# Performance work log

Measured on AMD Instinct MI355X. Metric: run time of the kernel, lower is better.

## Reference

```python
import jax, jax.numpy as jnp
import numpy as np

N = 1024
T = 8
HID = 256
FD = 64
SB = 8  # agents per sub-batch
EPS = 1e-6


def setup_inputs() -> dict:
    key = jax.random.key(0)
    ks = jax.random.split(key, 12)
    s = 0.05
    starts = jnp.arange(0, N, SB)
    sub_batches = jnp.stack([starts, starts + SB], axis=1).astype(jnp.int64)  # [128,2]
    return {
        'in_xy': jax.random.normal(ks[0], (T, N, 2), jnp.float32),
        'in_dxdy': jax.random.normal(ks[1], (T, N, 2), jnp.float32),
        'enc_h': jax.random.normal(ks[2], (N, HID), jnp.float32),
        'sub_batches': sub_batches,
        'W1': jax.random.normal(ks[3], (3, 32), jnp.float32) * s,
        'b1': jnp.zeros((32,), jnp.float32),
        'W2': jax.random.normal(ks[4], (32, 64), jnp.float32) * s,
        'b2': jnp.zeros((64,), jnp.float32),
        'W3': jax.random.normal(ks[5], (64, FD), jnp.float32) * s,
        'b3': jnp.zeros((FD,), jnp.float32),
        'Wa': jax.random.normal(ks[6], (HID, FD), jnp.float32) * s,
        'ba': jnp.zeros((FD,), jnp.float32),
    }


def _social_attention(in_xy, in_dxdy, enc_h, sub_batches, W1, b1, W2, b2, W3, b3, Wa, ba):
    x4 = jnp.concatenate([in_xy[-1], in_dxdy[-1]], axis=-1)  # [N,4] pos+vel
    # pairwise differences Dx[i,j] = x[i] - x[j]
    D = x4[:, None, :] - x4[None, :, :]                      # [N,N,4]
    Dp, Dv = D[..., :2], D[..., 2:]
    l2 = jnp.linalg.norm(Dp, axis=2)                         # [N,N]
    v = x4[:, 2:]                                            # [N,2] velocity of i
    dot_dp_v = Dp[..., 0] * v[:, None, 0] + Dp[..., 1] * v[:, None, 1]
    cos_theta = dot_dp_v / (l2 * jnp.linalg.norm(v, axis=1)[:, None] + EPS)
    dot_pv = jnp.sum(Dp * Dv, axis=-1)
    dv_sq = jnp.sum(Dv * Dv, axis=-1) + EPS
    ttca = -dot_pv / dv_sq
    dca = jnp.linalg.norm(Dp + ttca[..., None] * Dv, axis=2)
    feats = jnp.stack([l2, cos_theta, dca], axis=-1)         # [N,N,3]
    # social feature embedding MLP 3->32->64->FD
    h1 = jax.nn.relu(feats @ W1 + b1)
    h2 = jax.nn.relu(h1 @ W2 + b2)
    f = h2 @ W3 + b3                                         # [N,N,FD]
    # attention pooling, segmented by sub-batches with masked diagonal
    Wh = enc_h @ Wa + ba                                     # [N,FD]
    sigma = jnp.einsum('ijf,jf->ij', f, Wh)                  # [N,N]
    n = enc_h.shape[0]
    idx = jnp.arange(n)
    seg_id = jnp.searchsorted(sub_batches[:, 0], idx, side='right') - 1  # [N]
    same_seg = seg_id[:, None] == seg_id[None, :]
    diag = idx[:, None] == idx[None, :]
    score = jnp.where(diag, jnp.float32(-1000.0), sigma)
    score = jnp.where(same_seg, score, -jnp.inf)
    att = jax.nn.softmax(score, axis=1)                      # [N,N]
    S = att @ enc_h                                          # [N,HID]
    sizes = sub_batches[:, 1] - sub_batches[:, 0]
    keep = (sizes[seg_id] > 1)[:, None]
    return jnp.where(keep, S, jnp.float32(0.0))


def reference(in_xy, in_dxdy, enc_h, sub_batches, W1, b1, W2, b2, W3, b3, Wa, ba):
    return _social_attention(in_xy, in_dxdy, enc_h, sub_batches,
                             W1, b1, W2, b2, W3, b3, Wa, ba)
```

## Files before the change

### kernel.cpp

```cpp
#include <hip/hip_runtime.h>
#include <math.h>

#define NN    1024
#define TT    8
#define HIDD  256
#define FDD   64
#define SBB   8
#define EPSF  1e-6f
#define W3PAD 68
#define GPAD  68

__global__ __launch_bounds__(512) void social_attn_kernel(
    const float* __restrict__ in_xy,
    const float* __restrict__ in_dxdy,
    const float* __restrict__ enc_h,
    const float* __restrict__ W1, const float* __restrict__ b1,
    const float* __restrict__ W2, const float* __restrict__ b2,
    const float* __restrict__ W3, const float* __restrict__ b3,
    const float* __restrict__ Wa, const float* __restrict__ ba,
    float* __restrict__ out)
{
    __shared__ float sW1[96];
    __shared__ float sb1[32];
    __shared__ float sW2[32 * 64];
    __shared__ float sb2[64];
    __shared__ float sb3[64];
    __shared__ float sW3P[64 * W3PAD];
    __shared__ float sEnc[SBB * HIDD];
    __shared__ float sWh[SBB * FDD];
    __shared__ float sG[SBB * GPAD];
    __shared__ float sG0[SBB];
    __shared__ float sPsig[SBB * 64];
    __shared__ float sAtt[64];
    __shared__ float sX4[SBB][4];

    const int t    = threadIdx.x;
    const int wv   = t >> 6;
    const int lane = t & 63;
    const int seg  = blockIdx.x;
    const int base = seg * SBB;

    if (t < 96)        sW1[t]        = W1[t];
    else if (t < 128)  sb1[t - 96]   = b1[t - 96];
    else if (t < 192)  sb2[t - 128]  = b2[t - 128];
    else if (t < 256)  sb3[t - 192]  = b3[t - 192];
    ((float4*)sW2)[t] = ((const float4*)W2)[t];
    #pragma unroll
    for (int k = 0; k < 8; ++k) {
        const int idx = t + k * 512;
        sW3P[(idx >> 6) * W3PAD + (idx & 63)] = W3[idx];
    }
    ((float4*)sEnc)[t] = ((const float4*)(enc_h + (size_t)base * HIDD))[t];
    if (t < SBB) {
        const int g = base + t;
        const float* xy   = in_xy   + (TT - 1) * NN * 2;
        const float* dxdy = in_dxdy + (TT - 1) * NN * 2;
        sX4[t][0] = xy[2 * g];
        sX4[t][1] = xy[2 * g + 1];
        sX4[t][2] = dxdy[2 * g];
        sX4[t][3] = dxdy[2 * g + 1];
    }
    __syncthreads();

    const int cs = lane >> 4, k4 = lane & 15;
    float4 wacc = make_float4(0.f, 0.f, 0.f, 0.f);
    #pragma unroll 8
    for (int c2 = 0; c2 < 64; ++c2) {
        const int c = cs * 64 + ((c2 + 8 * cs) & 63);
        const float  e  = sEnc[wv * HIDD + c];
        const float4 wa = *(const float4*)&Wa[c * FDD + k4 * 4];
        wacc.x = fmaf(e, wa.x, wacc.x);
        wacc.y = fmaf(e, wa.y, wacc.y);
        wacc.z = fmaf(e, wa.z, wacc.z);
        wacc.w = fmaf(e, wa.w, wacc.w);
    }
    wacc.x += __shfl_xor(wacc.x, 16, 64);
    wacc.y += __shfl_xor(wacc.y, 16, 64);
    wacc.z += __shfl_xor(wacc.z, 16, 64);
    wacc.w += __shfl_xor(wacc.w, 16, 64);
    wacc.x += __shfl_xor(wacc.x, 32, 64);
    wacc.y += __shfl_xor(wacc.y, 32, 64);
    wacc.z += __shfl_xor(wacc.z, 32, 64);
    wacc.w += __shfl_xor(wacc.w, 32, 64);
    if (lane < 16) {
        const float4 bav = *(const float4*)&ba[k4 * 4];
        wacc.x += bav.x; wacc.y += bav.y; wacc.z += bav.z; wacc.w += bav.w;
        *(float4*)&sWh[wv * FDD + k4 * 4] = wacc;
    }

    float gacc = 0.f;
    #pragma unroll
    for (int c4 = 0; c4 < 16; ++c4) {
        const float4 w3 = *(const float4*)&sW3P[lane * W3PAD + c4 * 4];
        const float4 wh = *(const float4*)&sWh[wv * FDD + c4 * 4];
        gacc = fmaf(w3.x, wh.x, gacc);
        gacc = fmaf(w3.y, wh.y, gacc);
        gacc = fmaf(w3.z, wh.z, gacc);
        gacc = fmaf(w3.w, wh.w, gacc);
    }
    sG[wv * GPAD + lane] = gacc;
    float g0p = sb3[lane] * sWh[wv * FDD + lane];
    #pragma unroll
    for (int d = 1; d < 64; d <<= 1) g0p += __shfl_xor(g0p, d, 64);
    if (lane == 0) sG0[wv] = g0p;

    const int p = lane, i = p >> 3, j = p & 7, u = wv;
    const float dpx = sX4[i][0] - sX4[j][0];
    const float dpy = sX4[i][1] - sX4[j][1];
    const float dvx = sX4[i][2] - sX4[j][2];
    const float dvy = sX4[i][3] - sX4[j][3];
    const float l2  = sqrtf(dpx * dpx + dpy * dpy);
    const float vx  = sX4[i][2], vy = sX4[i][3];
    const float vnorm = sqrtf(vx * vx + vy * vy);
    const float cos_theta = (dpx * vx + dpy * vy) / (l2 * vnorm + EPSF);
    const float dot_pv = dpx * dvx + dpy * dvy;
    const float dv_sq  = dvx * dvx + dvy * dvy + EPSF;
    const float ttca   = -dot_pv / dv_sq;
    const float ex = dpx + ttca * dvx;
    const float ey = dpy + ttca * dvy;
    const float dca = sqrtf(ex * ex + ey * ey);

    float h1[32];
    #pragma unroll
    for (int c = 0; c < 32; ++c) {
        float a = sb1[c];
        a = fmaf(l2,        sW1[c],      a);
        a = fmaf(cos_theta, sW1[32 + c], a);
        a = fmaf(dca,       sW1[64 + c], a);
        h1[c] = a > 0.f ? a : 0.f;
    }

    float f2[8];
    #pragma unroll
    for (int cc = 0; cc < 8; ++cc) f2[cc] = sb2[u * 8 + cc];
    #pragma unroll
    for (int r = 0; r < 32; ++r) {
        const float hr = h1[r];
        const float4 wa = *(const float4*)&sW2[r * 64 + u * 8];
        const float4 wb = *(const float4*)&sW2[r * 64 + u * 8 + 4];
        f2[0] = fmaf(hr, wa.x, f2[0]);
        f2[1] = fmaf(hr, wa.y, f2[1]);
        f2[2] = fmaf(hr, wa.z, f2[2]);
        f2[3] = fmaf(hr, wa.w, f2[3]);
        f2[4] = fmaf(hr, wb.x, f2[4]);
        f2[5] = fmaf(hr, wb.y, f2[5]);
        f2[6] = fmaf(hr, wb.z, f2[6]);
        f2[7] = fmaf(hr, wb.w, f2[7]);
    }
    #pragma unroll
    for (int cc = 0; cc < 8; ++cc) f2[cc] = fmaxf(f2[cc], 0.f);
    __syncthreads();

    const float4 ga = *(const float4*)&sG[j * GPAD + u * 8];
    const float4 gb = *(const float4*)&sG[j * GPAD + u * 8 + 4];
    float psig;
    psig = f2[0] * ga.x;
    psig = fmaf(f2[1], ga.y, psig);
    psig = fmaf(f2[2], ga.z, psig);
    psig = fmaf(f2[3], ga.w, psig);
    psig = fmaf(f2[4], gb.x, psig);
    psig = fmaf(f2[5], gb.y, psig);
    psig = fmaf(f2[6], gb.z, psig);
    psig = fmaf(f2[7], gb.w, psig);
    sPsig[u * 64 + p] = psig;
    __syncthreads();

    float tot = sG0[j];
    #pragma unroll
    for (int uu = 0; uu < 8; ++uu) tot += sPsig[uu * 64 + lane];
    const float score = (i == j) ? -1000.f : tot;
    float m = score;
    m = fmaxf(m, __shfl_xor(m, 1, 64));
    m = fmaxf(m, __shfl_xor(m, 2, 64));
    m = fmaxf(m, __shfl_xor(m, 4, 64));
    const float e = expf(score - m);
    float ssum = e;
    ssum += __shfl_xor(ssum, 1, 64);
    ssum += __shfl_xor(ssum, 2, 64);
    ssum += __shfl_xor(ssum, 4, 64);
    if (t < 64) sAtt[lane] = e / ssum;
    __syncthreads();

    float4 acc4 = make_float4(0.f, 0.f, 0.f, 0.f);
    #pragma unroll
    for (int j2 = 0; j2 < 8; ++j2) {
        const float  a  = sAtt[wv * 8 + j2];
        const float4 ev = *(const float4*)&sEnc[j2 * HIDD + lane * 4];
        acc4.x = fmaf(a, ev.x, acc4.x);
        acc4.y = fmaf(a, ev.y, acc4.y);
        acc4.z = fmaf(a, ev.z, acc4.z);
        acc4.w = fmaf(a, ev.w, acc4.w);
    }
    *(float4*)&out[(size_t)(base + wv) * HIDD + lane * 4] = acc4;
}

extern "C" void kernel_launch(void* const* d_in, const int* in_sizes, int n_in,
                              void* d_out, int out_size, void* d_ws, size_t ws_size,
                              hipStream_t stream) {
    const float* in_xy   = (const float*)d_in[0];
    const float* in_dxdy = (const float*)d_in[1];
    const float* enc_h   = (const float*)d_in[2];
    const float* W1 = (const float*)d_in[4];
    const float* b1 = (const float*)d_in[5];
    const float* W2 = (const float*)d_in[6];
    const float* b2 = (const float*)d_in[7];
    const float* W3 = (const float*)d_in[8];
    const float* b3 = (const float*)d_in[9];
    const float* Wa = (const float*)d_in[10];
    const float* ba = (const float*)d_in[11];

    social_attn_kernel<<<NN / SBB, 512, 0, stream>>>(
        in_xy, in_dxdy, enc_h, W1, b1, W2, b2, W3, b3, Wa, ba, (float*)d_out);
}
```

Before: 13.97 us.

## Give each wave one query agent so scoring and softmax stay in registers

Work is remapped so each wave owns one query agent i. Lanes hold the neighbour j and a chunk of eight output channels, and the sigma reduction uses intra-wave shuffles instead of a shared-memory partial-sum array. This removes two __syncthreads barriers and the sPsig/sAtt shared buffers, and attention weights are broadcast with __shfl. Wh is also computed by reading enc_h directly from global memory before the first barrier, so it can overlap the shared-memory staging. In exchange, every wave now recomputes the pairwise features and the 3->32 MLP layer, and the Wh loop makes uncoalesced global reads.

After: 15.12 us. +8.2%, slower.

```diff
diff --git a/kernel.cpp b/kernel.cpp
--- a/kernel.cpp
+++ b/kernel.cpp
@@ -30,8 +30,6 @@
     __shared__ float sWh[SBB * FDD];
     __shared__ float sG[SBB * GPAD];
     __shared__ float sG0[SBB];
-    __shared__ float sPsig[SBB * 64];
-    __shared__ float sAtt[64];
     __shared__ float sX4[SBB][4];
 
     const int t    = threadIdx.x;
@@ -60,51 +58,58 @@
         sX4[t][2] = dxdy[2 * g];
         sX4[t][3] = dxdy[2 * g + 1];
     }
+
+    {
+        const int cs = lane >> 4, k4 = lane & 15;
+        const float* encq = enc_h + (size_t)(base + wv) * HIDD + cs * 64;
+        float4 wacc = make_float4(0.f, 0.f, 0.f, 0.f);
+        #pragma unroll 8
+        for (int c2 = 0; c2 < 64; ++c2) {
+            const float  e  = encq[c2];
+            const float4 wa = *(const float4*)&Wa[(cs * 64 + c2) * FDD + k4 * 4];
+            wacc.x = fmaf(e, wa.x, wacc.x);
+            wacc.y = fmaf(e, wa.y, wacc.y);
+            wacc.z = fmaf(e, wa.z, wacc.z);
+            wacc.w = fmaf(e, wa.w, wacc.w);
+        }
+        wacc.x += __shfl_xor(wacc.x, 16, 64);
+        wacc.y += __shfl_xor(wacc.y, 16, 64);
+        wacc.z += __shfl_xor(wacc.z, 16, 64);
+        wacc.w += __shfl_xor(wacc.w, 16, 64);
+        wacc.x += __shfl_xor(wacc.x, 32, 64);
+        wacc.y += __shfl_xor(wacc.y, 32, 64);
+        wacc.z += __shfl_xor(wacc.z, 32, 64);
+        wacc.w += __shfl_xor(wacc.w, 32, 64);
+        if (lane < 16) {
+            const float4 bav = *(const float4*)&ba[k4 * 4];
+            wacc.x += bav.x; wacc.y += bav.y; wacc.z += bav.z; wacc.w += bav.w;
+            *(float4*)&sWh[wv * FDD + k4 * 4] = wacc;
+        }
+    }
     __syncthreads();
 
-    const int cs = lane >> 4, k4 = lane & 15;
-    float4 wacc = make_float4(0.f, 0.f, 0.f, 0.f);
-    #pragma unroll 8
-    for (int c2 = 0; c2 < 64; ++c2) {
-        const int c = cs * 64 + ((c2 + 8 * cs) & 63);
-        const float  e  = sEnc[wv * HIDD + c];
-        const float4 wa = *(const float4*)&Wa[c * FDD + k4 * 4];
-        wacc.x = fmaf(e, wa.x, wacc.x);
-        wacc.y = fmaf(e, wa.y, wacc.y);
-        wacc.z = fmaf(e, wa.z, wacc.z);
-        wacc.w = fmaf(e, wa.w, wacc.w);
-    }
-    wacc.x += __shfl_xor(wacc.x, 16, 64);
-    wacc.y += __shfl_xor(wacc.y, 16, 64);
-    wacc.z += __shfl_xor(wacc.z, 16, 64);
-    wacc.w += __shfl_xor(wacc.w, 16, 64);
-    wacc.x += __shfl_xor(wacc.x, 32, 64);
-    wacc.y += __shfl_xor(wacc.y, 32, 64);
-    wacc.z += __shfl_xor(wacc.z, 32, 64);
-    wacc.w += __shfl_xor(wacc.w, 32, 64);
-    if (lane < 16) {
-        const float4 bav = *(const float4*)&ba[k4 * 4];
-        wacc.x += bav.x; wacc.y += bav.y; wacc.z += bav.z; wacc.w += bav.w;
-        *(float4*)&sWh[wv * FDD + k4 * 4] = wacc;
-    }
-
-    float gacc = 0.f;
-    #pragma unroll
-    for (int c4 = 0; c4 < 16; ++c4) {
-        const float4 w3 = *(const float4*)&sW3P[lane * W3PAD + c4 * 4];
-        const float4 wh = *(const float4*)&sWh[wv * FDD + c4 * 4];
-        gacc = fmaf(w3.x, wh.x, gacc);
-        gacc = fmaf(w3.y, wh.y, gacc);
-        gacc = fmaf(w3.z, wh.z, gacc);
-        gacc = fmaf(w3.w, wh.w, gacc);
-    }
-    sG[wv * GPAD + lane] = gacc;
-    float g0p = sb3[lane] * sWh[wv * FDD + lane];
-    #pragma unroll
-    for (int d = 1; d < 64; d <<= 1) g0p += __shfl_xor(g0p, d, 64);
-    if (lane == 0) sG0[wv] = g0p;
-
-    const int p = lane, i = p >> 3, j = p & 7, u = wv;
+    {
+        float gacc = 0.f;
+        #pragma unroll
+        for (int c4 = 0; c4 < 16; ++c4) {
+            const float4 w3 = *(const float4*)&sW3P[lane * W3PAD + c4 * 4];
+            const float4 wh = *(const float4*)&sWh[wv * FDD + c4 * 4];
+            gacc = fmaf(w3.x, wh.x, gacc);
+            gacc = fmaf(w3.y, wh.y, gacc);
+            gacc = fmaf(w3.z, wh.z, gacc);
+            gacc = fmaf(w3.w, wh.w, gacc);
+        }
+        sG[wv * GPAD + lane] = gacc;
+        float g0p = sb3[lane] * sWh[wv * FDD + lane];
+        #pragma unroll
+        for (int d = 1; d < 64; d <<= 1) g0p += __shfl_xor(g0p, d, 64);
+        if (lane == 0) sG0[wv] = g0p;
+    }
+
+    const int pp = lane >> 3;
+    const int cc = lane & 7;
+    const int i  = wv, j = pp;
+
     const float dpx = sX4[i][0] - sX4[j][0];
     const float dpy = sX4[i][1] - sX4[j][1];
     const float dvx = sX4[i][2] - sX4[j][2];
@@ -132,12 +137,12 @@
 
     float f2[8];
     #pragma unroll
-    for (int cc = 0; cc < 8; ++cc) f2[cc] = sb2[u * 8 + cc];
+    for (int k = 0; k < 8; ++k) f2[k] = sb2[cc * 8 + k];
     #pragma unroll
     for (int r = 0; r < 32; ++r) {
         const float hr = h1[r];
-        const float4 wa = *(const float4*)&sW2[r * 64 + u * 8];
-        const float4 wb = *(const float4*)&sW2[r * 64 + u * 8 + 4];
+        const float4 wa = *(const float4*)&sW2[r * 64 + cc * 8];
+        const float4 wb = *(const float4*)&sW2[r * 64 + cc * 8 + 4];
         f2[0] = fmaf(hr, wa.x, f2[0]);
         f2[1] = fmaf(hr, wa.y, f2[1]);
         f2[2] = fmaf(hr, wa.z, f2[2]);
@@ -148,43 +153,43 @@
         f2[7] = fmaf(hr, wb.w, f2[7]);
     }
     #pragma unroll
-    for (int cc = 0; cc < 8; ++cc) f2[cc] = fmaxf(f2[cc], 0.f);
+    for (int k = 0; k < 8; ++k) f2[k] = fmaxf(f2[k], 0.f);
     __syncthreads();
 
-    const float4 ga = *(const float4*)&sG[j * GPAD + u * 8];
-    const float4 gb = *(const float4*)&sG[j * GPAD + u * 8 + 4];
-    float psig;
-    psig = f2[0] * ga.x;
-    psig = fmaf(f2[1], ga.y, psig);
-    psig = fmaf(f2[2], ga.z, psig);
-    psig = fmaf(f2[3], ga.w, psig);
-    psig = fmaf(f2[4], gb.x, psig);
-    psig = fmaf(f2[5], gb.y, psig);
-    psig = fmaf(f2[6], gb.z, psig);
-    psig = fmaf(f2[7], gb.w, psig);
-    sPsig[u * 64 + p] = psig;
-    __syncthreads();
-
-    float tot = sG0[j];
-    #pragma unroll
-    for (int uu = 0; uu < 8; ++uu) tot += sPsig[uu * 64 + lane];
-    const float score = (i == j) ? -1000.f : tot;
+    float sig;
+    {
+        const float4 ga = *(const float4*)&sG[pp * GPAD + cc * 8];
+        const float4 gb = *(const float4*)&sG[pp * GPAD + cc * 8 + 4];
+        sig = f2[0] * ga.x;
+        sig = fmaf(f2[1], ga.y, sig);
+        sig = fmaf(f2[2], ga.z, sig);
+        sig = fmaf(f2[3], ga.w, sig);
+        sig = fmaf(f2[4], gb.x, sig);
+        sig = fmaf(f2[5], gb.y, sig);
+        sig = fmaf(f2[6], gb.z, sig);
+        sig = fmaf(f2[7], gb.w, sig);
+    }
+    sig += __shfl_xor(sig, 1, 64);
+    sig += __shfl_xor(sig, 2, 64);
+    sig += __shfl_xor(sig, 4, 64);
+    sig += sG0[pp];
+
+    const float score = (i == j) ? -1000.f : sig;
     float m = score;
-    m = fmaxf(m, __shfl_xor(m, 1, 64));
-    m = fmaxf(m, __shfl_xor(m, 2, 64));
-    m = fmaxf(m, __shfl_xor(m, 4, 64));
+    m = fmaxf(m, __shfl_xor(m, 8, 64));
+    m = fmaxf(m, __shfl_xor(m, 16, 64));
+    m = fmaxf(m, __shfl_xor(m, 32, 64));
     const float e = expf(score - m);
     float ssum = e;
-    ssum += __shfl_xor(ssum, 1, 64);
-    ssum += __shfl_xor(ssum, 2, 64);
-    ssum += __shfl_xor(ssum, 4, 64);
-    if (t < 64) sAtt[lane] = e / ssum;
-    __syncthreads();
+    ssum += __shfl_xor(ssum, 8, 64);
+    ssum += __shfl_xor(ssum, 16, 64);
+    ssum += __shfl_xor(ssum, 32, 64);
+    const float att = e / ssum;
 
     float4 acc4 = make_float4(0.f, 0.f, 0.f, 0.f);
     #pragma unroll
     for (int j2 = 0; j2 < 8; ++j2) {
-        const float  a  = sAtt[wv * 8 + j2];
+        const float a = __shfl(att, j2 * 8, 64);
         const float4 ev = *(const float4*)&sEnc[j2 * HIDD + lane * 4];
         acc4.x = fmaf(a, ev.x, acc4.x);
         acc4.y = fmaf(a, ev.y, acc4.y);
```

## Drop softmax max, fold bias term into psig, broadcast attention via readlane

Applied to the files above, without the earlier changes.

Every wave now computes the attention weights redundantly and broadcasts them with readlane, which removes the sAtt shared buffer and one block barrier. The softmax max-subtraction is dropped, which assumes scores stay small enough that expf cannot overflow. The b3·Wh term is folded into each wave's partial psig instead of a separate 64-lane shuffle reduction. W1 and b1 are packed into float4 rows and W3 is loaded with float4 vectors to cut load instructions.

Measured after the change: 14.33 us. 1.03x slower.

```diff
diff --git a/kernel.cpp b/kernel.cpp
--- a/kernel.cpp
+++ b/kernel.cpp
@@ -9,6 +9,7 @@
 #define EPSF  1e-6f
 #define W3PAD 68
 #define GPAD  68
+#define WHSTR 68
 
 __global__ __launch_bounds__(512) void social_attn_kernel(
     const float* __restrict__ in_xy,
@@ -20,18 +21,15 @@
     const float* __restrict__ Wa, const float* __restrict__ ba,
     float* __restrict__ out)
 {
-    __shared__ float sW1[96];
-    __shared__ float sb1[32];
+    __shared__ float sW1T[32 * 4];
     __shared__ float sW2[32 * 64];
     __shared__ float sb2[64];
     __shared__ float sb3[64];
     __shared__ float sW3P[64 * W3PAD];
     __shared__ float sEnc[SBB * HIDD];
-    __shared__ float sWh[SBB * FDD];
+    __shared__ float sWh[SBB * WHSTR];
     __shared__ float sG[SBB * GPAD];
-    __shared__ float sG0[SBB];
     __shared__ float sPsig[SBB * 64];
-    __shared__ float sAtt[64];
     __shared__ float sX4[SBB][4];
 
     const int t    = threadIdx.x;
@@ -40,15 +38,23 @@
     const int seg  = blockIdx.x;
     const int base = seg * SBB;
 
-    if (t < 96)        sW1[t]        = W1[t];
-    else if (t < 128)  sb1[t - 96]   = b1[t - 96];
-    else if (t < 192)  sb2[t - 128]  = b2[t - 128];
-    else if (t < 256)  sb3[t - 192]  = b3[t - 192];
+    if (t < 32) {
+        sW1T[t * 4]     = W1[t];
+        sW1T[t * 4 + 1] = W1[32 + t];
+        sW1T[t * 4 + 2] = W1[64 + t];
+        sW1T[t * 4 + 3] = b1[t];
+    } else if (t < 96)   sb2[t - 32] = b2[t - 32];
+    else if (t < 160)    sb3[t - 96] = b3[t - 96];
     ((float4*)sW2)[t] = ((const float4*)W2)[t];
-    #pragma unroll
-    for (int k = 0; k < 8; ++k) {
-        const int idx = t + k * 512;
-        sW3P[(idx >> 6) * W3PAD + (idx & 63)] = W3[idx];
+    {
+        const float4* W3v = (const float4*)W3;
+        #pragma unroll
+        for (int k = 0; k < 2; ++k) {
+            const int g   = t + k * 512;
+            const int row = g >> 4;
+            const int c4  = (g & 15) * 4;
+            *(float4*)&sW3P[row * W3PAD + c4] = W3v[g];
+        }
     }
     ((float4*)sEnc)[t] = ((const float4*)(enc_h + (size_t)base * HIDD))[t];
     if (t < SBB) {
@@ -62,47 +68,47 @@
     }
     __syncthreads();
 
-    const int cs = lane >> 4, k4 = lane & 15;
-    float4 wacc = make_float4(0.f, 0.f, 0.f, 0.f);
-    #pragma unroll 8
-    for (int c2 = 0; c2 < 64; ++c2) {
-        const int c = cs * 64 + ((c2 + 8 * cs) & 63);
-        const float  e  = sEnc[wv * HIDD + c];
-        const float4 wa = *(const float4*)&Wa[c * FDD + k4 * 4];
-        wacc.x = fmaf(e, wa.x, wacc.x);
-        wacc.y = fmaf(e, wa.y, wacc.y);
-        wacc.z = fmaf(e, wa.z, wacc.z);
-        wacc.w = fmaf(e, wa.w, wacc.w);
-    }
-    wacc.x += __shfl_xor(wacc.x, 16, 64);
-    wacc.y += __shfl_xor(wacc.y, 16, 64);
-    wacc.z += __shfl_xor(wacc.z, 16, 64);
-    wacc.w += __shfl_xor(wacc.w, 16, 64);
-    wacc.x += __shfl_xor(wacc.x, 32, 64);
-    wacc.y += __shfl_xor(wacc.y, 32, 64);
-    wacc.z += __shfl_xor(wacc.z, 32, 64);
-    wacc.w += __shfl_xor(wacc.w, 32, 64);
-    if (lane < 16) {
-        const float4 bav = *(const float4*)&ba[k4 * 4];
-        wacc.x += bav.x; wacc.y += bav.y; wacc.z += bav.z; wacc.w += bav.w;
-        *(float4*)&sWh[wv * FDD + k4 * 4] = wacc;
-    }
-
-    float gacc = 0.f;
-    #pragma unroll
-    for (int c4 = 0; c4 < 16; ++c4) {
-        const float4 w3 = *(const float4*)&sW3P[lane * W3PAD + c4 * 4];
-        const float4 wh = *(const float4*)&sWh[wv * FDD + c4 * 4];
-        gacc = fmaf(w3.x, wh.x, gacc);
-        gacc = fmaf(w3.y, wh.y, gacc);
-        gacc = fmaf(w3.z, wh.z, gacc);
-        gacc = fmaf(w3.w, wh.w, gacc);
-    }
-    sG[wv * GPAD + lane] = gacc;
-    float g0p = sb3[lane] * sWh[wv * FDD + lane];
-    #pragma unroll
-    for (int d = 1; d < 64; d <<= 1) g0p += __shfl_xor(g0p, d, 64);
-    if (lane == 0) sG0[wv] = g0p;
+    {
+        const int cs = lane >> 4, k4 = lane & 15;
+        float4 wacc = make_float4(0.f, 0.f, 0.f, 0.f);
+        #pragma unroll 8
+        for (int c2 = 0; c2 < 64; ++c2) {
+            const int c = cs * 64 + ((c2 + 8 * cs) & 63);
+            const float  e  = sEnc[wv * HIDD + c];
+            const float4 wa = *(const float4*)&Wa[(size_t)c * FDD + k4 * 4];
+            wacc.x = fmaf(e, wa.x, wacc.x);
+            wacc.y = fmaf(e, wa.y, wacc.y);
+            wacc.z = fmaf(e, wa.z, wacc.z);
+            wacc.w = fmaf(e, wa.w, wacc.w);
+        }
+        wacc.x += __shfl_xor(wacc.x, 16, 64);
+        wacc.y += __shfl_xor(wacc.y, 16, 64);
+        wacc.z += __shfl_xor(wacc.z, 16, 64);
+        wacc.w += __shfl_xor(wacc.w, 16, 64);
+        wacc.x += __shfl_xor(wacc.x, 32, 64);
+        wacc.y += __shfl_xor(wacc.y, 32, 64);
+        wacc.z += __shfl_xor(wacc.z, 32, 64);
+        wacc.w += __shfl_xor(wacc.w, 32, 64);
+        if (lane < 16) {
+            const float4 bav = *(const float4*)&ba[k4 * 4];
+            wacc.x += bav.x; wacc.y += bav.y; wacc.z += bav.z; wacc.w += bav.w;
+            *(float4*)&sWh[wv * WHSTR + k4 * 4] = wacc;
+        }
+    }
+
+    {
+        float gacc = 0.f;
+        #pragma unroll
+        for (int c4 = 0; c4 < 16; ++c4) {
+            const float4 w3 = *(const float4*)&sW3P[lane * W3PAD + c4 * 4];
+            const float4 wx = *(const float4*)&sWh[wv * WHSTR + c4 * 4];
+            gacc = fmaf(w3.x, wx.x, gacc);
+            gacc = fmaf(w3.y, wx.y, gacc);
+            gacc = fmaf(w3.z, wx.z, gacc);
+            gacc = fmaf(w3.w, wx.w, gacc);
+        }
+        sG[wv * GPAD + lane] = gacc;
+    }
 
     const int p = lane, i = p >> 3, j = p & 7, u = wv;
     const float dpx = sX4[i][0] - sX4[j][0];
@@ -123,10 +129,11 @@
     float h1[32];
     #pragma unroll
     for (int c = 0; c < 32; ++c) {
-        float a = sb1[c];
-        a = fmaf(l2,        sW1[c],      a);
-        a = fmaf(cos_theta, sW1[32 + c], a);
-        a = fmaf(dca,       sW1[64 + c], a);
+        const float4 w = *(const float4*)&sW1T[c * 4];
+        float a = w.w;
+        a = fmaf(l2,        w.x, a);
+        a = fmaf(cos_theta, w.y, a);
+        a = fmaf(dca,       w.z, a);
         h1[c] = a > 0.f ? a : 0.f;
     }
 
@@ -151,40 +158,50 @@
     for (int cc = 0; cc < 8; ++cc) f2[cc] = fmaxf(f2[cc], 0.f);
     __syncthreads();
 
-    const float4 ga = *(const float4*)&sG[j * GPAD + u * 8];
-    const float4 gb = *(const float4*)&sG[j * GPAD + u * 8 + 4];
-    float psig;
-    psig = f2[0] * ga.x;
-    psig = fmaf(f2[1], ga.y, psig);
-    psig = fmaf(f2[2], ga.z, psig);
-    psig = fmaf(f2[3], ga.w, psig);
-    psig = fmaf(f2[4], gb.x, psig);
-    psig = fmaf(f2[5], gb.y, psig);
-    psig = fmaf(f2[6], gb.z, psig);
-    psig = fmaf(f2[7], gb.w, psig);
-    sPsig[u * 64 + p] = psig;
+    {
+        const float4 ga  = *(const float4*)&sG[j * GPAD + u * 8];
+        const float4 gb  = *(const float4*)&sG[j * GPAD + u * 8 + 4];
+        const float4 wha = *(const float4*)&sWh[j * WHSTR + u * 8];
+        const float4 whb = *(const float4*)&sWh[j * WHSTR + u * 8 + 4];
+        const float4 b3a = *(const float4*)&sb3[u * 8];
+        const float4 b3b = *(const float4*)&sb3[u * 8 + 4];
+        float psig;
+        psig = f2[0] * ga.x;
+        psig = fmaf(f2[1], ga.y, psig);
+        psig = fmaf(f2[2], ga.z, psig);
+        psig = fmaf(f2[3], ga.w, psig);
+        psig = fmaf(f2[4], gb.x, psig);
+        psig = fmaf(f2[5], gb.y, psig);
+        psig = fmaf(f2[6], gb.z, psig);
+        psig = fmaf(f2[7], gb.w, psig);
+        psig = fmaf(b3a.x, wha.x, psig);
+        psig = fmaf(b3a.y, wha.y, psig);
+        psig = fmaf(b3a.z, wha.z, psig);
+        psig = fmaf(b3a.w, wha.w, psig);
+        psig = fmaf(b3b.x, whb.x, psig);
+        psig = fmaf(b3b.y, whb.y, psig);
+        psig = fmaf(b3b.z, whb.z, psig);
+        psig = fmaf(b3b.w, whb.w, psig);
+        sPsig[u * 64 + p] = psig;
+    }
     __syncthreads();
 
-    float tot = sG0[j];
+    float tot = 0.f;
     #pragma unroll
     for (int uu = 0; uu < 8; ++uu) tot += sPsig[uu * 64 + lane];
     const float score = (i == j) ? -1000.f : tot;
-    float m = score;
-    m = fmaxf(m, __shfl_xor(m, 1, 64));
-    m = fmaxf(m, __shfl_xor(m, 2, 64));
-    m = fmaxf(m, __shfl_xor(m, 4, 64));
-    const float e = expf(score - m);
+    const float e = expf(score);
     float ssum = e;
     ssum += __shfl_xor(ssum, 1, 64);
     ssum += __shfl_xor(ssum, 2, 64);
     ssum += __shfl_xor(ssum, 4, 64);
-    if (t < 64) sAtt[lane] = e / ssum;
-    __syncthreads();
+    const float att = e / ssum;
 
     float4 acc4 = make_float4(0.f, 0.f, 0.f, 0.f);
     #pragma unroll
     for (int j2 = 0; j2 < 8; ++j2) {
-        const float  a  = sAtt[wv * 8 + j2];
+        const float a = __int_as_float(
+            __builtin_amdgcn_readlane(__float_as_int(att), wv * 8 + j2));
         const float4 ev = *(const float4*)&sEnc[j2 * HIDD + lane * 4];
         acc4.x = fmaf(a, ev.x, acc4.x);
         acc4.y = fmaf(a, ev.y, acc4.y);
```
